# Kernel optimization log

Hardware: AMD Instinct MI355X
Metric: run time of the kernel (lower is better)

## Reference

```python
import jax, jax.numpy as jnp
import numpy as np

EPS = 1e-9
CLAMP_MAX = 5.0


def _mlp(x, W1, b1, W2, b2, W3, b3):
    h = jax.nn.relu(x @ W1.T + b1)
    h = jax.nn.relu(h @ W2.T + b2)
    return h @ W3.T + b3  # [B, C] logits


def _sem_loss_hierarchy(p, assoc_idx, assoc_mask, neg_assoc_idx, neg_assoc_mask):
    # p: [B, C] sigmoid probabilities.
    # For each class i: _s1 = clamp(sum_{k in assoc(i)} log(p_k + eps), max=5)
    #                   _s2 = clamp(sum_{k in neg_assoc(i)} log(1 - p_k + eps), max=5)
    # The original loop does s = clamp(s + exp(_s), max=1) sequentially; since every
    # exp(_s) > 0 this is exactly min(sum_i exp(_s_i), 1).
    logp = jnp.log(p + EPS)          # [B, C]
    log1mp = jnp.log(1.0 - p + EPS)  # [B, C]
    am = assoc_mask.astype(p.dtype)      # [C, A]
    nm = neg_assoc_mask.astype(p.dtype)  # [C, NA]
    # gather per-class association sets: [B, C, A] / [B, C, NA]
    s1_in = (logp[:, assoc_idx] * am).sum(-1)        # [B, C]
    s2_in = (log1mp[:, neg_assoc_idx] * nm).sum(-1)  # [B, C]
    s1 = jnp.minimum(jnp.exp(jnp.minimum(s1_in, CLAMP_MAX)).sum(-1), 1.0)  # [B]
    s2 = jnp.minimum(jnp.exp(jnp.minimum(s2_in, CLAMP_MAX)).sum(-1), 1.0)  # [B]
    return (-jnp.log(s1) - jnp.log(s2)).mean()


def setup_inputs() -> dict:
    key = jax.random.key(0)
    ks = jax.random.split(key, 12)
    B, Bu, C, A, NA, D = 1024, 1024, 1024, 32, 64, 28 * 28
    x = jax.random.normal(ks[0], (B, D), dtype=jnp.float32)
    x_unlab = jax.random.normal(ks[1], (Bu, D), dtype=jnp.float32)
    y = jax.random.randint(ks[2], (B,), 0, C)
    assoc_idx = jax.random.randint(ks[3], (C, A), 0, C, dtype=jnp.int32)
    neg_assoc_idx = jax.random.randint(ks[4], (C, NA), 0, C, dtype=jnp.int32)
    assoc_mask = jnp.ones((C, A), dtype=bool)
    neg_assoc_mask = jnp.ones((C, NA), dtype=bool)
    W1 = jax.random.normal(ks[5], (512, D), dtype=jnp.float32) * 0.02
    b1 = jnp.zeros((512,), dtype=jnp.float32)
    W2 = jax.random.normal(ks[6], (128, 512), dtype=jnp.float32) * 0.02
    b2 = jnp.zeros((128,), dtype=jnp.float32)
    W3 = jax.random.normal(ks[7], (C, 128), dtype=jnp.float32) * 0.02
    b3 = jnp.zeros((C,), dtype=jnp.float32)
    return {"x": x, "y": y, "x_unlab": x_unlab, "assoc_idx": assoc_idx,
            "assoc_mask": assoc_mask, "neg_assoc_idx": neg_assoc_idx,
            "neg_assoc_mask": neg_assoc_mask, "W1": W1, "b1": b1,
            "W2": W2, "b2": b2, "W3": W3, "b3": b3}


def reference(x, y, x_unlab, assoc_idx, assoc_mask, neg_assoc_idx,
              neg_assoc_mask, W1, b1, W2, b2, W3, b3):
    C = W3.shape[0]
    out = _mlp(x, W1, b1, W2, b2, W3, b3)  # [B, C]
    target = jax.nn.one_hot(y, C, dtype=out.dtype)  # pack_y
    # BCEWithLogitsLoss (mean over all elements): softplus(z) - t*z
    ce = jnp.mean(jax.nn.softplus(out) - out * target)
    sl_lab = _sem_loss_hierarchy(jax.nn.sigmoid(out), assoc_idx, assoc_mask,
                                 neg_assoc_idx, neg_assoc_mask)
    out_u = _mlp(x_unlab, W1, b1, W2, b2, W3, b3)
    sl_unlab = _sem_loss_hierarchy(jax.nn.sigmoid(out_u), assoc_idx, assoc_mask,
                                   neg_assoc_idx, neg_assoc_mask)
    loss = ce
    sl = sl_lab + sl_unlab
    return loss, sl
```

## Files before the change

### kernel.cpp

```cpp
#include <hip/hip_runtime.h>
#include <math.h>

#define B_LAB 1024
#define B_TOT 2048
#define CDIM  1024
#define DDIM  784
#define DPAD  832
#define H1DIM 512
#define H2DIM 128

typedef __attribute__((ext_vector_type(8))) __bf16 bf16x8;
typedef __attribute__((ext_vector_type(4))) float f32x4;
typedef __attribute__((ext_vector_type(8))) unsigned short ushort8;

#define OFF_XB    0u
#define OFF_W1B   3407872u
#define OFF_H1B   4259840u
#define OFF_LPB   0u
#define OFF_L1PB  4194304u
#define OFF_MAB   8388608u
#define OFF_MNB   10485760u
#define OFF_W2B   12582912u
#define OFF_W3B   12713984u
#define OFF_H2B   12976128u
#define OFF_ROWS  13500416u

__device__ __forceinline__ unsigned short f2bf(float f) {
    unsigned int u = __builtin_bit_cast(unsigned int, f);
    u = (u + 0x7fff + ((u >> 16) & 1)) >> 16;
    return (unsigned short)u;
}

__device__ __forceinline__ void gload_lds16(const void* g, void* l) {
    __builtin_amdgcn_global_load_lds(
        (const __attribute__((address_space(1))) unsigned int*)g,
        (__attribute__((address_space(3))) unsigned int*)l, 16, 0, 0);
}

__global__ __launch_bounds__(256) void prep(
    const int* __restrict__ aidx, const int* __restrict__ nidx,
    const float* __restrict__ x, const float* __restrict__ xu,
    const float* __restrict__ W1, const float* __restrict__ W2,
    const float* __restrict__ W3,
    unsigned short* __restrict__ Mab, unsigned short* __restrict__ Mnb,
    unsigned short* __restrict__ XB, unsigned short* __restrict__ W1B,
    unsigned short* __restrict__ W2B, unsigned short* __restrict__ W3B,
    float* __restrict__ zero_base)
{
    __shared__ int cnt[2 * CDIM];
    const int bid = blockIdx.x, tid = threadIdx.x;

    if (bid < 1024) {
        const int i = bid;
        for (int j = tid; j < 2 * CDIM; j += 256) cnt[j] = 0;
        __syncthreads();
        if (tid < 32)       atomicAdd(&cnt[aidx[i * 32 + tid]], 1);
        else if (tid < 96)  atomicAdd(&cnt[CDIM + nidx[i * 64 + (tid - 32)]], 1);
        __syncthreads();
        for (int j = tid; j < CDIM; j += 256) {
            Mab[(size_t)i * CDIM + j] = f2bf((float)cnt[j]);
            Mnb[(size_t)i * CDIM + j] = f2bf((float)cnt[CDIM + j]);
        }
        return;
    }
    if (bid < 2160) {
        const float* src; unsigned short* dst; int K, cpr, chunk;
        if (bid < 1856) {
            int b = bid - 1024;
            bool lab = (b < 416);
            src = lab ? x : xu;
            dst = XB + (lab ? (size_t)0 : (size_t)B_LAB * DPAD);
            K = DDIM; cpr = 104;
            chunk = (lab ? b : b - 416) * 256 + tid;
        } else if (bid < 2064) {
            src = W1; dst = W1B; K = DDIM; cpr = 104;
            chunk = (bid - 1856) * 256 + tid;
        } else if (bid < 2096) {
            src = W2; dst = W2B; K = H1DIM; cpr = 64;
            chunk = (bid - 2064) * 256 + tid;
        } else {
            src = W3; dst = W3B; K = H2DIM; cpr = 16;
            chunk = (bid - 2096) * 256 + tid;
        }
        int row = chunk / cpr;
        int col = (chunk - row * cpr) * 8;
        int Kp  = cpr * 8;
        ushort8 o = {};
        if (col < K) {
            const float4* s = (const float4*)(src + (size_t)row * K + col);
            float4 a = s[0], b4 = s[1];
            o[0] = f2bf(a.x);  o[1] = f2bf(a.y);  o[2] = f2bf(a.z);  o[3] = f2bf(a.w);
            o[4] = f2bf(b4.x); o[5] = f2bf(b4.y); o[6] = f2bf(b4.z); o[7] = f2bf(b4.w);
        }
        *(ushort8*)(dst + (size_t)row * Kp + col) = o;
        return;
    }
    int base = (bid - 2160) * 2048 + tid * 8;
    #pragma unroll
    for (int k = 0; k < 8; ++k) {
        int j = base + k;
        if (j < 2 * B_TOT + 2) zero_base[j] = 0.f;
    }
}

template <int RELU>
__global__ __launch_bounds__(256) void mfma_gemm(
    const unsigned short* __restrict__ A, const unsigned short* __restrict__ W,
    const float* __restrict__ bias, unsigned short* __restrict__ out,
    int M, int N, int K)
{
    __shared__ __align__(16) char smem[2][16384];

    const int tid  = threadIdx.x;
    const int lane = tid & 63;
    const int w    = tid >> 6;
    const int wr   = w >> 1, wc = w & 1;
    const int lr   = lane & 15, lg = lane >> 4;
    const int m0   = blockIdx.y * 64;
    const int n0   = blockIdx.x * 64;
    const int NT   = K >> 6;

    f32x4 acc[2][2] = {};

    auto stage = [&](int b, int kt) {
        char* As = smem[b];
        char* Bs = smem[b] + 8192;
        #pragma unroll
        for (int l = 0; l < 2; ++l) {
            int d   = (l * 256 + tid) << 4;
            int row = d >> 7;
            int e   = d ^ ((row & 7) << 4);
            int col = (e & 127) >> 1;
            gload_lds16(A + (size_t)(m0 + row) * K + kt * 64 + col, As + d);
            gload_lds16(W + (size_t)(n0 + row) * K + kt * 64 + col, Bs + d);
        }
    };

    stage(0, 0);
    __syncthreads();

    int cur = 0;
    for (int kt = 0; kt < NT; ++kt) {
        if (kt + 1 < NT) stage(cur ^ 1, kt + 1);
        char* As = smem[cur];
        char* Bs = smem[cur] + 8192;
        #pragma unroll
        for (int ks = 0; ks < 2; ++ks) {
            bf16x8 af[2], bfv[2];
            #pragma unroll
            for (int mi = 0; mi < 2; ++mi) {
                int r = wr * 32 + mi * 16 + lr;
                af[mi] = *(const bf16x8*)(As + r * 128 +
                          ((ks * 64 + lg * 16) ^ ((r & 7) << 4)));
            }
            #pragma unroll
            for (int ni = 0; ni < 2; ++ni) {
                int r = wc * 32 + ni * 16 + lr;
                bfv[ni] = *(const bf16x8*)(Bs + r * 128 +
                          ((ks * 64 + lg * 16) ^ ((r & 7) << 4)));
            }
            #pragma unroll
            for (int mi = 0; mi < 2; ++mi)
                #pragma unroll
                for (int ni = 0; ni < 2; ++ni)
                    acc[mi][ni] = __builtin_amdgcn_mfma_f32_16x16x32_bf16(
                        af[mi], bfv[ni], acc[mi][ni], 0, 0, 0);
        }
        __syncthreads();
        cur ^= 1;
    }

    #pragma unroll
    for (int mi = 0; mi < 2; ++mi)
        #pragma unroll
        for (int r = 0; r < 4; ++r) {
            int m = m0 + wr * 32 + mi * 16 + lg * 4 + r;
            #pragma unroll
            for (int ni = 0; ni < 2; ++ni) {
                int n = n0 + wc * 32 + ni * 16 + lr;
                float v = acc[mi][ni][r] + bias[n];
                if (RELU) v = fmaxf(v, 0.f);
                out[(size_t)m * N + n] = f2bf(v);
            }
        }
}

__global__ __launch_bounds__(256) void gemm3_fused(
    const unsigned short* __restrict__ A, const unsigned short* __restrict__ W,
    const float* __restrict__ bias, const int* __restrict__ y,
    unsigned short* __restrict__ LPb, unsigned short* __restrict__ L1Pb,
    float* __restrict__ ce_acc)
{
    __shared__ __align__(16) char smem[2][16384];
    __shared__ float part[4];

    const int tid  = threadIdx.x;
    const int lane = tid & 63;
    const int w    = tid >> 6;
    const int wr   = w >> 1, wc = w & 1;
    const int lr   = lane & 15, lg = lane >> 4;
    const int m0   = blockIdx.y * 64;
    const int n0   = blockIdx.x * 64;
    const int NT   = H2DIM >> 6;

    f32x4 acc[2][2] = {};

    auto stage = [&](int b, int kt) {
        char* As = smem[b];
        char* Bs = smem[b] + 8192;
        #pragma unroll
        for (int l = 0; l < 2; ++l) {
            int d   = (l * 256 + tid) << 4;
            int row = d >> 7;
            int e   = d ^ ((row & 7) << 4);
            int col = (e & 127) >> 1;
            gload_lds16(A + (size_t)(m0 + row) * H2DIM + kt * 64 + col, As + d);
            gload_lds16(W + (size_t)(n0 + row) * H2DIM + kt * 64 + col, Bs + d);
        }
    };

    stage(0, 0);
    __syncthreads();

    int cur = 0;
    for (int kt = 0; kt < NT; ++kt) {
        if (kt + 1 < NT) stage(cur ^ 1, kt + 1);
        char* As = smem[cur];
        char* Bs = smem[cur] + 8192;
        #pragma unroll
        for (int ks = 0; ks < 2; ++ks) {
            bf16x8 af[2], bfv[2];
            #pragma unroll
            for (int mi = 0; mi < 2; ++mi) {
                int r = wr * 32 + mi * 16 + lr;
                af[mi] = *(const bf16x8*)(As + r * 128 +
                          ((ks * 64 + lg * 16) ^ ((r & 7) << 4)));
            }
            #pragma unroll
            for (int ni = 0; ni < 2; ++ni) {
                int r = wc * 32 + ni * 16 + lr;
                bfv[ni] = *(const bf16x8*)(Bs + r * 128 +
                          ((ks * 64 + lg * 16) ^ ((r & 7) << 4)));
            }
            #pragma unroll
            for (int mi = 0; mi < 2; ++mi)
                #pragma unroll
                for (int ni = 0; ni < 2; ++ni)
                    acc[mi][ni] = __builtin_amdgcn_mfma_f32_16x16x32_bf16(
                        af[mi], bfv[ni], acc[mi][ni], 0, 0, 0);
        }
        __syncthreads();
        cur ^= 1;
    }

    const bool lab = (m0 < B_LAB);
    float ce_local = 0.f;
    #pragma unroll
    for (int mi = 0; mi < 2; ++mi)
        #pragma unroll
        for (int r = 0; r < 4; ++r) {
            int m = m0 + wr * 32 + mi * 16 + lg * 4 + r;
            int tgt = lab ? y[m] : -1;
            #pragma unroll
            for (int ni = 0; ni < 2; ++ni) {
                int n = n0 + wc * 32 + ni * 16 + lr;
                float z  = acc[mi][ni][r] + bias[n];
                float sp = fmaxf(z, 0.f) + log1pf(expf(-fabsf(z)));
                LPb[(size_t)m * CDIM + n]  = f2bf(z - sp);
                L1Pb[(size_t)m * CDIM + n] = f2bf(-sp);
                if (lab) ce_local += (n == tgt) ? (sp - z) : sp;
            }
        }
    if (lab) {
        for (int off = 32; off; off >>= 1) ce_local += __shfl_down(ce_local, off);
        if ((tid & 63) == 0) part[tid >> 6] = ce_local;
        __syncthreads();
        if (tid == 0)
            atomicAdd(ce_acc, part[0] + part[1] + part[2] + part[3]);
    }
}

__global__ __launch_bounds__(256) void sem_gemm(
    const unsigned short* __restrict__ LPb, const unsigned short* __restrict__ L1Pb,
    const unsigned short* __restrict__ Mab, const unsigned short* __restrict__ Mnb,
    float* __restrict__ rows1, float* __restrict__ rows2)
{
    __shared__ __align__(16) char smem[2][16384];

    const unsigned short* Ag = (blockIdx.z == 0) ? LPb : L1Pb;
    const unsigned short* Bg = (blockIdx.z == 0) ? Mab : Mnb;
    float* rows = (blockIdx.z == 0) ? rows1 : rows2;

    const int tid  = threadIdx.x;
    const int lane = tid & 63;
    const int w    = tid >> 6;
    const int wr   = w >> 1, wc = w & 1;
    const int lr   = lane & 15, lg = lane >> 4;
    const int m0   = blockIdx.y * 64;
    const int n0   = blockIdx.x * 64;
    const int NT   = CDIM >> 6;

    f32x4 acc[2][2] = {};

    auto stage = [&](int b, int kt) {
        char* As = smem[b];
        char* Bs = smem[b] + 8192;
        #pragma unroll
        for (int l = 0; l < 2; ++l) {
            int d   = (l * 256 + tid) << 4;
            int row = d >> 7;
            int e   = d ^ ((row & 7) << 4);
            int col = (e & 127) >> 1;
            gload_lds16(Ag + (size_t)(m0 + row) * CDIM + kt * 64 + col, As + d);
            gload_lds16(Bg + (size_t)(n0 + row) * CDIM + kt * 64 + col, Bs + d);
        }
    };

    stage(0, 0);
    __syncthreads();

    int cur = 0;
    for (int kt = 0; kt < NT; ++kt) {
        if (kt + 1 < NT) stage(cur ^ 1, kt + 1);
        char* As = smem[cur];
        char* Bs = smem[cur] + 8192;
        #pragma unroll
        for (int ks = 0; ks < 2; ++ks) {
            bf16x8 af[2], bfv[2];
            #pragma unroll
            for (int mi = 0; mi < 2; ++mi) {
                int r = wr * 32 + mi * 16 + lr;
                af[mi] = *(const bf16x8*)(As + r * 128 +
                          ((ks * 64 + lg * 16) ^ ((r & 7) << 4)));
            }
            #pragma unroll
            for (int ni = 0; ni < 2; ++ni) {
                int r = wc * 32 + ni * 16 + lr;
                bfv[ni] = *(const bf16x8*)(Bs + r * 128 +
                          ((ks * 64 + lg * 16) ^ ((r & 7) << 4)));
            }
            #pragma unroll
            for (int mi = 0; mi < 2; ++mi)
                #pragma unroll
                for (int ni = 0; ni < 2; ++ni)
                    acc[mi][ni] = __builtin_amdgcn_mfma_f32_16x16x32_bf16(
                        af[mi], bfv[ni], acc[mi][ni], 0, 0, 0);
        }
        __syncthreads();
        cur ^= 1;
    }

    #pragma unroll
    for (int mi = 0; mi < 2; ++mi) {
        #pragma unroll
        for (int r = 0; r < 4; ++r) {
            float s = expf(fminf(acc[mi][0][r], 5.f))
                    + expf(fminf(acc[mi][1][r], 5.f));
            s += __shfl_xor(s, 1);
            s += __shfl_xor(s, 2);
            s += __shfl_xor(s, 4);
            s += __shfl_xor(s, 8);
            if (lr == 0) {
                int m = m0 + wr * 32 + mi * 16 + lg * 4 + r;
                atomicAdd(&rows[m], s);
            }
        }
    }
}

__global__ __launch_bounds__(256) void final_kernel(
    const float* __restrict__ rows1, const float* __restrict__ rows2,
    const float* __restrict__ ce_acc, float* __restrict__ out)
{
    __shared__ float part[4];
    float s = 0.f;
    for (int i = threadIdx.x; i < B_TOT; i += 256)
        s += -logf(fminf(rows1[i], 1.f)) - logf(fminf(rows2[i], 1.f));
    for (int off = 32; off; off >>= 1) s += __shfl_down(s, off);
    if ((threadIdx.x & 63) == 0) part[threadIdx.x >> 6] = s;
    __syncthreads();
    if (threadIdx.x == 0) {
        out[1] = (part[0] + part[1] + part[2] + part[3]) * (1.f / (float)B_LAB);
        out[0] = ce_acc[0] * (1.f / ((float)B_LAB * (float)CDIM));
    }
}

extern "C" void kernel_launch(void* const* d_in, const int* in_sizes, int n_in,
                              void* d_out, int out_size, void* d_ws, size_t ws_size,
                              hipStream_t stream)
{
    const float* x    = (const float*)d_in[0];
    const int*   y    = (const int*)  d_in[1];
    const float* xu   = (const float*)d_in[2];
    const int*   aidx = (const int*)  d_in[3];
    const int*   nidx = (const int*)  d_in[5];
    const float* W1 = (const float*)d_in[7];
    const float* b1 = (const float*)d_in[8];
    const float* W2 = (const float*)d_in[9];
    const float* b2 = (const float*)d_in[10];
    const float* W3 = (const float*)d_in[11];
    const float* b3 = (const float*)d_in[12];

    char* ws = (char*)d_ws;
    unsigned short* XB   = (unsigned short*)(ws + OFF_XB);
    unsigned short* W1B  = (unsigned short*)(ws + OFF_W1B);
    unsigned short* H1B  = (unsigned short*)(ws + OFF_H1B);
    unsigned short* LPb  = (unsigned short*)(ws + OFF_LPB);
    unsigned short* L1Pb = (unsigned short*)(ws + OFF_L1PB);
    unsigned short* MAB  = (unsigned short*)(ws + OFF_MAB);
    unsigned short* MNB  = (unsigned short*)(ws + OFF_MNB);
    unsigned short* W2B  = (unsigned short*)(ws + OFF_W2B);
    unsigned short* W3B  = (unsigned short*)(ws + OFF_W3B);
    unsigned short* H2B  = (unsigned short*)(ws + OFF_H2B);
    float* ROWS = (float*)(ws + OFF_ROWS);
    float* ACC  = ROWS + 2 * B_TOT;
    float* out  = (float*)d_out;

    prep<<<2163, 256, 0, stream>>>(aidx, nidx, x, xu, W1, W2, W3,
                                   MAB, MNB, XB, W1B, W2B, W3B, ROWS);

    mfma_gemm<1><<<dim3(H1DIM / 64, B_TOT / 64), 256, 0, stream>>>(
        XB, W1B, b1, H1B, B_TOT, H1DIM, DPAD);
    mfma_gemm<1><<<dim3(H2DIM / 64, B_TOT / 64), 256, 0, stream>>>(
        H1B, W2B, b2, H2B, B_TOT, H2DIM, H1DIM);
    gemm3_fused<<<dim3(CDIM / 64, B_TOT / 64), 256, 0, stream>>>(
        H2B, W3B, b3, y, LPb, L1Pb, ACC);

    sem_gemm<<<dim3(CDIM / 64, B_TOT / 64, 2), 256, 0, stream>>>(
        LPb, L1Pb, MAB, MNB, ROWS, ROWS + B_TOT);
    final_kernel<<<1, 256, 0, stream>>>(ROWS, ROWS + B_TOT, ACC, out);
}
```

Measured before the change: 61.79 us.

## Widen sem_gemm N tile to 128 and fuse final reduction via last-block counter

Each sem_gemm block now covers 128 columns of the association matrix instead of 64, doubling per-block work and B-tile reuse of the A tile. The separate final_kernel launch is removed: blocks increment a global counter after their atomics, and the last block reads the row sums atomically and writes both outputs. This saves a kernel launch and reduces A-tile reloads, but adds LDS/register pressure and depends on the counter being zero at entry.

```diff
diff --git a/kernel.cpp b/kernel.cpp
--- a/kernel.cpp
+++ b/kernel.cpp
@@ -8,6 +8,8 @@
 #define DPAD  832
 #define H1DIM 512
 #define H2DIM 128
+
+#define SEM_BLOCKS 512
 
 typedef __attribute__((ext_vector_type(8))) __bf16 bf16x8;
 typedef __attribute__((ext_vector_type(4))) float f32x4;
@@ -283,9 +285,12 @@
 __global__ __launch_bounds__(256) void sem_gemm(
     const unsigned short* __restrict__ LPb, const unsigned short* __restrict__ L1Pb,
     const unsigned short* __restrict__ Mab, const unsigned short* __restrict__ Mnb,
-    float* __restrict__ rows1, float* __restrict__ rows2)
+    float* __restrict__ rows1, float* __restrict__ rows2,
+    float* __restrict__ acc2 , float* __restrict__ out)
 {
-    __shared__ __align__(16) char smem[2][16384];
+    __shared__ __align__(16) char smem[2][24576];
+    __shared__ float part[4];
+    __shared__ int lastflag;
 
     const unsigned short* Ag = (blockIdx.z == 0) ? LPb : L1Pb;
     const unsigned short* Bg = (blockIdx.z == 0) ? Mab : Mnb;
@@ -297,10 +302,10 @@
     const int wr   = w >> 1, wc = w & 1;
     const int lr   = lane & 15, lg = lane >> 4;
     const int m0   = blockIdx.y * 64;
-    const int n0   = blockIdx.x * 64;
+    const int n0   = blockIdx.x * 128;
     const int NT   = CDIM >> 6;
 
-    f32x4 acc[2][2] = {};
+    f32x4 acc[2][4] = {};
 
     auto stage = [&](int b, int kt) {
         char* As = smem[b];
@@ -312,6 +317,13 @@
             int e   = d ^ ((row & 7) << 4);
             int col = (e & 127) >> 1;
             gload_lds16(Ag + (size_t)(m0 + row) * CDIM + kt * 64 + col, As + d);
+        }
+        #pragma unroll
+        for (int l = 0; l < 4; ++l) {
+            int d   = (l * 256 + tid) << 4;
+            int row = d >> 7;
+            int e   = d ^ ((row & 7) << 4);
+            int col = (e & 127) >> 1;
             gload_lds16(Bg + (size_t)(n0 + row) * CDIM + kt * 64 + col, Bs + d);
         }
     };
@@ -326,7 +338,7 @@
         char* Bs = smem[cur] + 8192;
         #pragma unroll
         for (int ks = 0; ks < 2; ++ks) {
-            bf16x8 af[2], bfv[2];
+            bf16x8 af[2], bfv[4];
             #pragma unroll
             for (int mi = 0; mi < 2; ++mi) {
                 int r = wr * 32 + mi * 16 + lr;
@@ -334,15 +346,15 @@
                           ((ks * 64 + lg * 16) ^ ((r & 7) << 4)));
             }
             #pragma unroll
-            for (int ni = 0; ni < 2; ++ni) {
-                int r = wc * 32 + ni * 16 + lr;
+            for (int ni = 0; ni < 4; ++ni) {
+                int r = wc * 64 + ni * 16 + lr;
                 bfv[ni] = *(const bf16x8*)(Bs + r * 128 +
                           ((ks * 64 + lg * 16) ^ ((r & 7) << 4)));
             }
             #pragma unroll
             for (int mi = 0; mi < 2; ++mi)
                 #pragma unroll
-                for (int ni = 0; ni < 2; ++ni)
+                for (int ni = 0; ni < 4; ++ni)
                     acc[mi][ni] = __builtin_amdgcn_mfma_f32_16x16x32_bf16(
                         af[mi], bfv[ni], acc[mi][ni], 0, 0, 0);
         }
@@ -354,8 +366,10 @@
     for (int mi = 0; mi < 2; ++mi) {
         #pragma unroll
         for (int r = 0; r < 4; ++r) {
-            float s = expf(fminf(acc[mi][0][r], 5.f))
-                    + expf(fminf(acc[mi][1][r], 5.f));
+            float s = 0.f;
+            #pragma unroll
+            for (int ni = 0; ni < 4; ++ni)
+                s += expf(fminf(acc[mi][ni][r], 5.f));
             s += __shfl_xor(s, 1);
             s += __shfl_xor(s, 2);
             s += __shfl_xor(s, 4);
@@ -366,22 +380,27 @@
             }
         }
     }
-}
-
-__global__ __launch_bounds__(256) void final_kernel(
-    const float* __restrict__ rows1, const float* __restrict__ rows2,
-    const float* __restrict__ ce_acc, float* __restrict__ out)
-{
-    __shared__ float part[4];
+
+    __threadfence();
+    if (tid == 0) {
+        unsigned old = atomicAdd((unsigned int*)(acc2 + 1), 1u);
+        lastflag = (old == SEM_BLOCKS - 1);
+    }
+    __syncthreads();
+    if (!lastflag) return;
+
     float s = 0.f;
-    for (int i = threadIdx.x; i < B_TOT; i += 256)
-        s += -logf(fminf(rows1[i], 1.f)) - logf(fminf(rows2[i], 1.f));
+    for (int i = tid; i < B_TOT; i += 256) {
+        float r1 = atomicAdd(&rows1[i], 0.f);
+        float r2 = atomicAdd(&rows2[i], 0.f);
+        s += -logf(fminf(r1, 1.f)) - logf(fminf(r2, 1.f));
+    }
     for (int off = 32; off; off >>= 1) s += __shfl_down(s, off);
-    if ((threadIdx.x & 63) == 0) part[threadIdx.x >> 6] = s;
+    if ((tid & 63) == 0) part[tid >> 6] = s;
     __syncthreads();
-    if (threadIdx.x == 0) {
+    if (tid == 0) {
         out[1] = (part[0] + part[1] + part[2] + part[3]) * (1.f / (float)B_LAB);
-        out[0] = ce_acc[0] * (1.f / ((float)B_LAB * (float)CDIM));
+        out[0] = atomicAdd(acc2, 0.f) * (1.f / ((float)B_LAB * (float)CDIM));
     }
 }
 
@@ -426,7 +445,6 @@
     gemm3_fused<<<dim3(CDIM / 64, B_TOT / 64), 256, 0, stream>>>(
         H2B, W3B, b3, y, LPb, L1Pb, ACC);
 
-    sem_gemm<<<dim3(CDIM / 64, B_TOT / 64, 2), 256, 0, stream>>>(
-        LPb, L1Pb, MAB, MNB, ROWS, ROWS + B_TOT);
-    final_kernel<<<1, 256, 0, stream>>>(ROWS, ROWS + B_TOT, ACC, out);
-}
+    sem_gemm<<<dim3(CDIM / 128, B_TOT / 64, 2), 256, 0, stream>>>(
+        LPb, L1Pb, MAB, MNB, ROWS, ROWS + B_TOT, ACC, out);
+}
```

Result: slower. 92.13 us (+49.1%).
